# Performance work log

Measured on AMD Instinct MI355X. Metric: run time of the kernel, lower is better.

Reference implementation:

```python
import jax, jax.numpy as jnp
import numpy as np

B, S, H, L, NH, DH, V, FF, WD, W = 16, 512, 768, 12, 12, 64, 30522, 3072, 256, 255
T = S - 1


def layer_norm(x, s, b, eps=1e-12):
    m = jnp.mean(x, -1, keepdims=True)
    v = jnp.mean((x - m) ** 2, -1, keepdims=True)
    return (x - m) * jax.lax.rsqrt(v + eps) * s + b


def setup_inputs() -> dict:
    key = jax.random.key(0)
    ks = jax.random.split(key, 20)
    rng = np.random.RandomState(0)
    # ragged structure: words per sentence and wordpieces per word
    sent_lens = rng.randint(128, W + 1, size=B)
    token_lens = np.zeros((B, W), dtype=np.int32)
    for i in range(B):
        token_lens[i, : sent_lens[i]] = rng.randint(1, 3, size=sent_lens[i])
    bert_len = token_lens.sum(1)  # wordpieces per sentence (no CLS/SEP)
    attention_mask = (np.arange(S)[None, :] < (bert_len + 2)[:, None]).astype(np.int32)
    input_ids = rng.randint(0, V, size=(B, S)).astype(np.int32)
    sd = 0.02
    rn = lambda k, sh: jax.random.normal(k, sh, jnp.float32) * sd
    inp = {
        "input_ids": jnp.asarray(input_ids),
        "attention_mask": jnp.asarray(attention_mask),
        "token_lens": jnp.asarray(token_lens),
        "word_emb": rn(ks[0], (V, H)),
        "pos_emb": rn(ks[1], (S, H)),
        "type_emb": rn(ks[2], (2, H)),
        "emb_ln_s": jnp.ones((H,), jnp.float32),
        "emb_ln_b": jnp.zeros((H,), jnp.float32),
        "Wq": rn(ks[3], (L, H, H)), "bq": jnp.zeros((L, H), jnp.float32),
        "Wk": rn(ks[4], (L, H, H)), "bk": jnp.zeros((L, H), jnp.float32),
        "Wv": rn(ks[5], (L, H, H)), "bv": jnp.zeros((L, H), jnp.float32),
        "Wo": rn(ks[6], (L, H, H)), "bo": jnp.zeros((L, H), jnp.float32),
        "ln1_s": jnp.ones((L, H), jnp.float32), "ln1_b": jnp.zeros((L, H), jnp.float32),
        "W1": rn(ks[7], (L, H, FF)), "b1": jnp.zeros((L, FF), jnp.float32),
        "W2": rn(ks[8], (L, FF, H)), "b2": jnp.zeros((L, H), jnp.float32),
        "ln2_s": jnp.ones((L, H), jnp.float32), "ln2_b": jnp.zeros((L, H), jnp.float32),
        "proj_W": rn(ks[9], (H, WD)), "proj_b": jnp.zeros((WD,), jnp.float32),
    }
    return inp


def reference(input_ids, attention_mask, token_lens, word_emb, pos_emb, type_emb,
              emb_ln_s, emb_ln_b, Wq, bq, Wk, bk, Wv, bv, Wo, bo, ln1_s, ln1_b,
              W1, b1, W2, b2, ln2_s, ln2_b, proj_W, proj_b):
    # --- BERT embeddings ---
    h = word_emb[input_ids] + pos_emb[None, :, :] + type_emb[0][None, None, :]
    h = layer_norm(h, emb_ln_s, emb_ln_b)
    att_bias = (1.0 - attention_mask.astype(jnp.float32))[:, None, None, :] * -10000.0

    def block(h, p):
        wq, bq_, wk, bk_, wv, bv_, wo, bo_, l1s, l1b, w1, b1_, w2, b2_, l2s, l2b = p
        q = (h @ wq + bq_).reshape(B, S, NH, DH)
        k = (h @ wk + bk_).reshape(B, S, NH, DH)
        v = (h @ wv + bv_).reshape(B, S, NH, DH)
        scores = jnp.einsum('bqnd,bknd->bnqk', q, k) / np.float32(np.sqrt(DH)) + att_bias
        a = jax.nn.softmax(scores, axis=-1)
        ctx = jnp.einsum('bnqk,bknd->bqnd', a, v).reshape(B, S, H)
        h = layer_norm(h + ctx @ wo + bo_, l1s, l1b)
        f = jax.nn.gelu(h @ w1 + b1_, approximate=False) @ w2 + b2_
        h = layer_norm(h + f, l2s, l2b)
        return h, None

    h, _ = jax.lax.scan(block, h, (Wq, bq, Wk, bk, Wv, bv, Wo, bo, ln1_s, ln1_b,
                                   W1, b1, W2, b2, ln2_s, ln2_b))
    # drop [CLS], project to word_dims
    hid = h[:, 1:, :] @ proj_W + proj_b  # [B, T, WD]
    # --- ragged segment-mean merge (vectorized form of merge_embedding) ---
    cum = jnp.cumsum(token_lens, axis=1)  # [B, W]
    pos = jnp.arange(T)
    word_id = jnp.sum(pos[None, :, None] >= cum[:, None, :], axis=-1)  # token -> word
    valid = pos[None, :] < cum[:, -1][:, None]  # token within bert_len
    onehot = ((word_id[:, :, None] == jnp.arange(W)[None, None, :]) & valid[:, :, None]).astype(hid.dtype)
    sums = jnp.einsum('btw,btd->bwd', onehot, hid)  # [B, W, WD]
    means = sums / jnp.maximum(token_lens, 1)[:, :, None].astype(hid.dtype)
    word_masks = (token_lens > 0).astype(jnp.float32)  # [B, W]
    return means, word_masks
```

## Files before the change

### kernel.cpp

```cpp
#include <hip/hip_runtime.h>
#include <stdint.h>

#define B_ 16
#define S_ 512
#define H_ 768
#define L_ 12
#define NH_ 12
#define DH_ 64
#define FF_ 3072
#define WD_ 256
#define W_ 255
#define MTOK_ (B_*S_)
#define QKVN_ 2304
#define MPADR_ 128

typedef _Float16 f16;
typedef _Float16 f16x8 __attribute__((ext_vector_type(8)));
typedef _Float16 f16x4 __attribute__((ext_vector_type(4)));
typedef _Float16 f16x2 __attribute__((ext_vector_type(2)));
typedef float f32x4 __attribute__((ext_vector_type(4)));

#define SCHED_FENCE() __builtin_amdgcn_sched_barrier(0)

__device__ __forceinline__ float gelu_fast(float x) {
  float u = x * (1.0f + 0.044715f * x * x);
  float e = __expf(-1.5957691216f * u);
  return __fdividef(x, 1.0f + e);
}

__device__ __forceinline__ void gload16(const f16* g, f16* l) {
  __builtin_amdgcn_global_load_lds(
      (const __attribute__((address_space(1))) void*)g,
      (__attribute__((address_space(3))) void*)l, 16, 0, 0);
}

template<int BM, int BN, int ACT, int OUTF16, int BIAS, int QKVW>
__global__ __launch_bounds__(256) void gemm2_k(
    const f16* __restrict__ A, const f16* __restrict__ Bm, void* __restrict__ Cv,
    const float* __restrict__ bias, f16* __restrict__ vTp,
    const int* __restrict__ rowmap, const int* __restrict__ meta,
    int lda, int ldb, int ldc, int K, float scale)
{
  constexpr int MI = BM / 32;
  constexpr int NI = BN / 32;
  constexpr int LPW = BM / 32 + BN / 32;
  const int gx = gridDim.x;
  int flat = blockIdx.y * gx + blockIdx.x;
  const int nlive = (meta[1] / BM) * gx;
  if (flat >= nlive) return;
  {
    int q = nlive >> 3, r = nlive & 7;
    int xcd = flat & 7, idx = flat >> 3;
    flat = (xcd < r ? xcd * (q + 1) : r * (q + 1) + (xcd - r) * q) + idx;
  }
  const int row0 = (flat / gx) * BM;
  const int col0 = (flat % gx) * BN;

  __shared__ __align__(16) f16 lA[2][BM * 64];
  __shared__ __align__(16) f16 lB[2][BN * 64];
  const int lane = threadIdx.x & 63;
  const int wave = threadIdx.x >> 6;
  const int wr = wave >> 1, wc = wave & 1;
  const int srow = lane >> 3;
  const int scol = lane & 7;
  const int cs = scol ^ srow;

  int arow[BM / 32];
#pragma unroll
  for (int i = 0; i < BM / 32; ++i)
    arow[i] = rowmap[row0 + (wave * (BM / 32) + i) * 8 + srow];

  auto stage = [&](int p, int k0) {
#pragma unroll
    for (int i = 0; i < BM / 32; ++i) {
      int seg = wave * (BM / 32) + i;
      gload16(&A[(size_t)arow[i] * lda + k0 + cs * 8], &lA[p][seg * 512]);
    }
#pragma unroll
    for (int i = 0; i < BN / 32; ++i) {
      int seg = wave * (BN / 32) + i;
      gload16(&Bm[(size_t)(col0 + seg * 8 + srow) * ldb + k0 + cs * 8], &lB[p][seg * 512]);
    }
  };

  f32x4 acc[MI][NI] = {};
  const int nt = K >> 6;
  const int rl = lane & 15, g = lane >> 4;
  stage(0, 0);
  if (nt > 1) stage(1, 64);
  for (int t = 0; t < nt; ++t) {
    if (t < nt - 1) { asm volatile("s_waitcnt vmcnt(%0) lgkmcnt(0)" :: "i"(LPW) : "memory"); }
    else            { asm volatile("s_waitcnt vmcnt(0) lgkmcnt(0)" ::: "memory"); }
    SCHED_FENCE();
    __builtin_amdgcn_s_barrier();
    SCHED_FENCE();
    const int p = t & 1;
    __builtin_amdgcn_s_setprio(1);
#pragma unroll
    for (int c = 0; c < 2; ++c) {
      f16x8 af[MI], bf[NI];
#pragma unroll
      for (int mi = 0; mi < MI; ++mi) {
        int r = wr * (MI * 16) + mi * 16 + rl;
        int u = (c * 4 + g) ^ (r & 7);
        af[mi] = *(const f16x8*)&lA[p][r * 64 + u * 8];
      }
#pragma unroll
      for (int ni = 0; ni < NI; ++ni) {
        int r = wc * (NI * 16) + ni * 16 + rl;
        int u = (c * 4 + g) ^ (r & 7);
        bf[ni] = *(const f16x8*)&lB[p][r * 64 + u * 8];
      }
#pragma unroll
      for (int mi = 0; mi < MI; ++mi)
#pragma unroll
        for (int ni = 0; ni < NI; ++ni)
          acc[mi][ni] = __builtin_amdgcn_mfma_f32_16x16x32_f16(af[mi], bf[ni], acc[mi][ni], 0, 0, 0);
    }
    __builtin_amdgcn_s_setprio(0);
    SCHED_FENCE();
    asm volatile("s_waitcnt lgkmcnt(0)" ::: "memory");
    SCHED_FENCE();
    __builtin_amdgcn_s_barrier();
    SCHED_FENCE();
    if (t + 2 < nt) stage(p, (t + 2) * 64);
  }
  const int cl = lane & 15;
  const int rq = (lane >> 4) * 4;
#pragma unroll
  for (int mi = 0; mi < MI; ++mi) {
    const int4 rm4 = *(const int4*)&rowmap[row0 + wr * (MI * 16) + mi * 16 + rq];
    const int rows[4] = { rm4.x, rm4.y, rm4.z, rm4.w };
    const bool contig = (rm4.w == rm4.x + 3) && ((rm4.x & 3) == 0);
#pragma unroll
    for (int ni = 0; ni < NI; ++ni) {
      int col = col0 + wc * (NI * 16) + ni * 16 + cl;
      float bv = 0.f;
      if constexpr (BIAS) bv = bias[col];
      if constexpr (QKVW) {
        if (col >= 2 * H_) {
          int vc = col - 2 * H_;
          int h = vc >> 6, d = vc & 63;
          if (contig) {
            if (rm4.x < MTOK_) {
              int b = rm4.x >> 9, s = rm4.x & (S_ - 1);
              f16x4 o4;
#pragma unroll
              for (int r = 0; r < 4; ++r) o4[r] = (f16)(acc[mi][ni][r] * scale + bv);
              *(f16x4*)&vTp[(((size_t)(b * NH_ + h)) * DH_ + d) * S_ + s] = o4;
            }
          } else {
#pragma unroll
            for (int r = 0; r < 4; ++r) {
              int orow = rows[r];
              if (orow < MTOK_) {
                int b = orow >> 9, s = orow & (S_ - 1);
                vTp[(((size_t)(b * NH_ + h)) * DH_ + d) * S_ + s] = (f16)(acc[mi][ni][r] * scale + bv);
              }
            }
          }
          continue;
        }
      }
#pragma unroll
      for (int r = 0; r < 4; ++r) {
        float v = acc[mi][ni][r] * scale + bv;
        if constexpr (ACT == 1) v = gelu_fast(v);
        if constexpr (OUTF16) {
          ((f16*)Cv)[(size_t)rows[r] * ldc + col] = (f16)v;
        } else {
          ((float*)Cv)[(size_t)rows[r] * ldc + col] = v;
        }
      }
    }
  }
}

__global__ __launch_bounds__(256) void fattn_k(
    const f16* __restrict__ qkv, const f16* __restrict__ vT,
    f16* __restrict__ ctx, const int* __restrict__ lenp)
{
  const int bh = blockIdx.x, qt = blockIdx.y;
  const int b = bh / NH_, h = bh - b * NH_;
  const int L = lenp[b];
  if ((qt << 7) >= L) return;
  const int nkt = (L + 63) >> 6;
  const int lane = threadIdx.x & 63, wave = threadIdx.x >> 6;
  const int rl = lane & 15, g = lane >> 4;
  const int srow = lane >> 3, scol = lane & 7;
  const int cs = scol ^ srow;

  __shared__ __align__(16) f16 lK[2][64 * 64];
  __shared__ __align__(16) f16 lV[2][64 * 64];
  __shared__ __align__(16) f16 lP[128 * 72];

  auto stage = [&](int p, int kt) {
#pragma unroll
    for (int i = 0; i < 2; ++i) {
      int seg = wave * 2 + i;
      int r = seg * 8 + srow;
      gload16(&qkv[((size_t)b * S_ + kt * 64 + r) * QKVN_ + H_ + h * DH_ + cs * 8], &lK[p][seg * 512]);
      gload16(&vT[((size_t)bh * DH_ + r) * S_ + kt * 64 + cs * 8], &lV[p][seg * 512]);
    }
  };

  const size_t qrow0 = (size_t)b * S_ + qt * 128 + wave * 32;
  f16x8 qf[2][2];
#pragma unroll
  for (int bq = 0; bq < 2; ++bq)
#pragma unroll
    for (int kc = 0; kc < 2; ++kc)
      qf[bq][kc] = *(const f16x8*)&qkv[(qrow0 + bq * 16 + rl) * QKVN_ + h * DH_ + kc * 32 + g * 8];

  float lsum[2] = {0.f, 0.f};
  f32x4 accO[2][4] = {};

  stage(0, 0);
  for (int kt = 0; kt < nkt; ++kt) {
    if (kt + 1 < nkt) {
      stage((kt + 1) & 1, kt + 1);
      asm volatile("s_waitcnt vmcnt(4) lgkmcnt(0)" ::: "memory");
    } else {
      asm volatile("s_waitcnt vmcnt(0) lgkmcnt(0)" ::: "memory");
    }
    SCHED_FENCE();
    __builtin_amdgcn_s_barrier();
    SCHED_FENCE();
    const int p = kt & 1;

    f32x4 accS[4][2] = {};
    __builtin_amdgcn_s_setprio(1);
#pragma unroll
    for (int kc = 0; kc < 2; ++kc) {
#pragma unroll
      for (int ak = 0; ak < 4; ++ak) {
        int row = ak * 16 + rl;
        int u = (kc * 4 + g) ^ (row & 7);
        f16x8 kf = *(const f16x8*)&lK[p][row * 64 + u * 8];
#pragma unroll
        for (int bq = 0; bq < 2; ++bq)
          accS[ak][bq] = __builtin_amdgcn_mfma_f32_16x16x32_f16(kf, qf[bq][kc], accS[ak][bq], 0, 0, 0);
      }
    }
    __builtin_amdgcn_s_setprio(0);

    const int kvb = kt * 64 + g * 4;
#pragma unroll
    for (int bq = 0; bq < 2; ++bq) {
      float pv[16];
      float ps = 0.f;
#pragma unroll
      for (int ak = 0; ak < 4; ++ak)
#pragma unroll
        for (int r = 0; r < 4; ++r) {
          float s = accS[ak][bq][r] * 0.125f;
          float pp = (kvb + ak * 16 + r < L) ? __expf(s) : 0.f;
          pv[ak * 4 + r] = pp;
          ps += pp;
        }
      ps += __shfl_xor(ps, 16);
      ps += __shfl_xor(ps, 32);
      lsum[bq] += ps;
      const int qrow = wave * 32 + bq * 16 + rl;
#pragma unroll
      for (int ak = 0; ak < 4; ++ak)
#pragma unroll
        for (int r2 = 0; r2 < 2; ++r2) {
          f16x2 pk = { (f16)pv[ak * 4 + r2 * 2], (f16)pv[ak * 4 + r2 * 2 + 1] };
          *(f16x2*)&lP[qrow * 72 + ak * 16 + g * 4 + r2 * 2] = pk;
        }
    }
    __builtin_amdgcn_s_setprio(1);
#pragma unroll
    for (int kc = 0; kc < 2; ++kc) {
      f16x8 pa[2], vf[4];
#pragma unroll
      for (int aq = 0; aq < 2; ++aq) {
        int prow = wave * 32 + aq * 16 + rl;
        pa[aq] = *(const f16x8*)&lP[prow * 72 + kc * 32 + g * 8];
      }
#pragma unroll
      for (int bd = 0; bd < 4; ++bd) {
        int vrow = bd * 16 + rl;
        int u = (kc * 4 + g) ^ (vrow & 7);
        vf[bd] = *(const f16x8*)&lV[p][vrow * 64 + u * 8];
      }
#pragma unroll
      for (int aq = 0; aq < 2; ++aq)
#pragma unroll
        for (int bd = 0; bd < 4; ++bd)
          accO[aq][bd] = __builtin_amdgcn_mfma_f32_16x16x32_f16(pa[aq], vf[bd], accO[aq][bd], 0, 0, 0);
    }
    __builtin_amdgcn_s_setprio(0);
    SCHED_FENCE();
    asm volatile("s_waitcnt lgkmcnt(0)" ::: "memory");
    SCHED_FENCE();
    __builtin_amdgcn_s_barrier();
    SCHED_FENCE();
  }

  float linv[2] = { 1.f / lsum[0], 1.f / lsum[1] };
  const size_t orow0 = (size_t)b * S_ + qt * 128 + wave * 32;
#pragma unroll
  for (int aq = 0; aq < 2; ++aq)
#pragma unroll
    for (int r = 0; r < 4; ++r) {
      float li = __shfl(linv[aq], (lane & 48) | (g * 4 + r));
      int q = aq * 16 + g * 4 + r;
#pragma unroll
      for (int bd = 0; bd < 4; ++bd)
        ctx[(orow0 + q) * H_ + h * DH_ + bd * 16 + rl] = (f16)(accO[aq][bd][r] * li);
    }
}

template<typename TI>
__global__ __launch_bounds__(256) void transpose_f16_k(
    const TI* __restrict__ in, f16* __restrict__ out,
    int ldin, int ldout, long i1, long o1)
{
  const int z = blockIdx.z;
  in  += (size_t)z * i1;
  out += (size_t)z * o1;
  __shared__ float t[32][33];
  const int kt = blockIdx.y * 32, nt = blockIdx.x * 32;
  const int tx = threadIdx.x & 31, tg = threadIdx.x >> 5;
#pragma unroll
  for (int i = 0; i < 4; ++i) {
    int k = tg * 4 + i;
    t[k][tx] = (float)in[(size_t)(kt + k) * ldin + nt + tx];
  }
  __syncthreads();
#pragma unroll
  for (int i = 0; i < 4; ++i) {
    int n = tg * 4 + i;
    out[(size_t)(nt + n) * ldout + kt + tx] = (f16)t[tx][n];
  }
}

__global__ void bias_cat_k(const float* __restrict__ bq, const float* __restrict__ bk,
                           const float* __restrict__ bv, float* __restrict__ out) {
  const int l = blockIdx.y;
  const int j = blockIdx.x * 256 + threadIdx.x;
  float v = (j < H_) ? bq[l * H_ + j] : (j < 2 * H_) ? bk[l * H_ + j - H_] : bv[l * H_ + j - 2 * H_];
  out[l * QKVN_ + j] = v;
}

__global__ __launch_bounds__(256) void embed_ln_k(
    const int* __restrict__ ids, const float* __restrict__ wemb,
    const float* __restrict__ pemb, const float* __restrict__ temb,
    const float* __restrict__ lns, const float* __restrict__ lnb,
    float* __restrict__ h32, f16* __restrict__ h16)
{
  const int row = blockIdx.x * 4 + (threadIdx.x >> 6);
  const int lane = threadIdx.x & 63;
  const int s = row & (S_ - 1);
  const float4* wp = (const float4*)(wemb + (size_t)ids[row] * H_);
  const float4* pp = (const float4*)(pemb + (size_t)s * H_);
  const float4* tp = (const float4*)temb;
  float4 x[3]; float sm = 0.f, sq = 0.f;
#pragma unroll
  for (int j = 0; j < 3; ++j) {
    int i4 = lane + 64 * j;
    float4 a = wp[i4], bb = pp[i4], c = tp[i4];
    float4 v; v.x = a.x + bb.x + c.x; v.y = a.y + bb.y + c.y;
    v.z = a.z + bb.z + c.z; v.w = a.w + bb.w + c.w;
    x[j] = v;
    sm += v.x + v.y + v.z + v.w;
    sq += v.x * v.x + v.y * v.y + v.z * v.z + v.w * v.w;
  }
#pragma unroll
  for (int o = 32; o > 0; o >>= 1) { sm += __shfl_xor(sm, o); sq += __shfl_xor(sq, o); }
  float mean = sm * (1.f / H_);
  float inv = rsqrtf(sq * (1.f / H_) - mean * mean + 1e-12f);
  float4* hw = (float4*)(h32 + (size_t)row * H_);
  f16* ho = h16 + (size_t)row * H_;
#pragma unroll
  for (int j = 0; j < 3; ++j) {
    int i4 = lane + 64 * j;
    float4 sc = ((const float4*)lns)[i4], bi = ((const float4*)lnb)[i4];
    float4 v = x[j], y;
    y.x = (v.x - mean) * inv * sc.x + bi.x;
    y.y = (v.y - mean) * inv * sc.y + bi.y;
    y.z = (v.z - mean) * inv * sc.z + bi.z;
    y.w = (v.w - mean) * inv * sc.w + bi.w;
    hw[i4] = y;
    f16x4 o4 = {(f16)y.x, (f16)y.y, (f16)y.z, (f16)y.w};
    *(f16x4*)&ho[i4 * 4] = o4;
  }
}

__global__ __launch_bounds__(256) void ln_res_k(
    float* __restrict__ h32, const f16* __restrict__ tmp,
    const float* __restrict__ lns, const float* __restrict__ lnb,
    f16* __restrict__ h16, const int* __restrict__ rowmap, const int* __restrict__ meta)
{
  const int crow = blockIdx.x * 4 + (threadIdx.x >> 6);
  if (crow >= meta[0]) return;
  const int row = rowmap[crow];
  const int lane = threadIdx.x & 63;
  const float4* hp = (const float4*)(h32 + (size_t)row * H_);
  const f16x4* tp = (const f16x4*)(tmp + (size_t)row * H_);
  float4 x[3]; float sm = 0.f, sq = 0.f;
#pragma unroll
  for (int j = 0; j < 3; ++j) {
    int i4 = lane + 64 * j;
    float4 a = hp[i4];
    f16x4 tv = tp[i4];
    float4 v; v.x = a.x + (float)tv[0]; v.y = a.y + (float)tv[1];
    v.z = a.z + (float)tv[2]; v.w = a.w + (float)tv[3];
    x[j] = v;
    sm += v.x + v.y + v.z + v.w;
    sq += v.x * v.x + v.y * v.y + v.z * v.z + v.w * v.w;
  }
#pragma unroll
  for (int o = 32; o > 0; o >>= 1) { sm += __shfl_xor(sm, o); sq += __shfl_xor(sq, o); }
  float mean = sm * (1.f / H_);
  float inv = rsqrtf(sq * (1.f / H_) - mean * mean + 1e-12f);
  float4* hw = (float4*)(h32 + (size_t)row * H_);
  f16* ho = h16 + (size_t)row * H_;
#pragma unroll
  for (int j = 0; j < 3; ++j) {
    int i4 = lane + 64 * j;
    float4 sc = ((const float4*)lns)[i4], bi = ((const float4*)lnb)[i4];
    float4 v = x[j], y;
    y.x = (v.x - mean) * inv * sc.x + bi.x;
    y.y = (v.y - mean) * inv * sc.y + bi.y;
    y.z = (v.z - mean) * inv * sc.z + bi.z;
    y.w = (v.w - mean) * inv * sc.w + bi.w;
    hw[i4] = y;
    f16x4 o4 = {(f16)y.x, (f16)y.y, (f16)y.z, (f16)y.w};
    *(f16x4*)&ho[i4 * 4] = o4;
  }
}

__global__ void len_k(const int* __restrict__ mask, int* __restrict__ len) {
  const int b = blockIdx.x;
  const int t = threadIdx.x;
  __shared__ int red[512];
  red[t] = mask[b * S_ + t]; __syncthreads();
  for (int o = 256; o > 0; o >>= 1) { if (t < o) red[t] += red[t + o]; __syncthreads(); }
  if (t == 0) len[b] = red[0];
}

__global__ void rowmap_k(const int* __restrict__ len, int* __restrict__ meta,
                         int* __restrict__ rowmap) {
  __shared__ int cum[17];
  if (threadIdx.x == 0) {
    int c = 0; cum[0] = 0;
    for (int b = 0; b < B_; ++b) { c += len[b]; cum[b + 1] = c; }
    meta[0] = c;
    meta[1] = (c + 127) & ~127;
  }
  __syncthreads();
  const int Mv = cum[16];
  for (int i = threadIdx.x; i < MTOK_ + MPADR_; i += 256) {
    int orig;
    if (i < Mv) {
      int b = 0;
#pragma unroll
      for (int t = 1; t <= 16; ++t) b += (i >= cum[t]) ? 1 : 0;
      orig = b * S_ + (i - cum[b]);
    } else {
      int d = i - Mv;
      orig = MTOK_ + (d < MPADR_ ? d : MPADR_ - 1);
    }
    rowmap[i] = orig;
  }
}

__global__ __launch_bounds__(256) void merge_k(
    const float* __restrict__ proj, const int* __restrict__ tl,
    float* __restrict__ means, float* __restrict__ masks)
{
  const int w = blockIdx.x, b = blockIdx.y;
  const int t = threadIdx.x;
  __shared__ int red[256];
  int part = 0;
  for (int j = t; j < w; j += 256) part += tl[b * W_ + j];
  red[t] = part; __syncthreads();
  for (int o = 128; o > 0; o >>= 1) { if (t < o) red[t] += red[t + o]; __syncthreads(); }
  const int start = red[0];
  const int len = tl[b * W_ + w];
  float s = 0.f;
  for (int l = 0; l < len; ++l)
    s += proj[((size_t)b * S_ + 1 + start + l) * WD_ + t];
  means[((size_t)b * W_ + w) * WD_ + t] = (len > 0) ? s / (float)len : 0.f;
  if (t == 0) masks[b * W_ + w] = (len > 0) ? 1.f : 0.f;
}

extern "C" void kernel_launch(void* const* d_in, const int* in_sizes, int n_in,
                              void* d_out, int out_size, void* d_ws, size_t ws_size,
                              hipStream_t stream)
{
  (void)in_sizes; (void)n_in; (void)out_size;
  const int*   ids   = (const int*)d_in[0];
  const int*   amask = (const int*)d_in[1];
  const int*   tlens = (const int*)d_in[2];
  const float* wemb  = (const float*)d_in[3];
  const float* pemb  = (const float*)d_in[4];
  const float* temb  = (const float*)d_in[5];
  const float* elns  = (const float*)d_in[6];
  const float* elnb  = (const float*)d_in[7];
  const float* Wq = (const float*)d_in[8];  const float* bq = (const float*)d_in[9];
  const float* Wk = (const float*)d_in[10]; const float* bk = (const float*)d_in[11];
  const float* Wv = (const float*)d_in[12]; const float* bv = (const float*)d_in[13];
  const float* Wo = (const float*)d_in[14]; const float* bo = (const float*)d_in[15];
  const float* l1s = (const float*)d_in[16]; const float* l1b = (const float*)d_in[17];
  const float* W1 = (const float*)d_in[18]; const float* b1 = (const float*)d_in[19];
  const float* W2 = (const float*)d_in[20]; const float* b2 = (const float*)d_in[21];
  const float* l2s = (const float*)d_in[22]; const float* l2b = (const float*)d_in[23];
  const float* pW = (const float*)d_in[24]; const float* pb = (const float*)d_in[25];

  const int MR = MTOK_ + MPADR_;
  char* ws = (char*)d_ws;
  size_t off = 0;
  auto alloc = [&](size_t n) { void* r = ws + off; off += (n + 255) & ~(size_t)255; return r; };
  float* h32   = (float*)alloc((size_t)MR * H_ * 4);
  f16*   h16   = (f16*)alloc((size_t)MR * H_ * 2);
  f16*   qkv   = (f16*)alloc((size_t)MR * QKVN_ * 2);
  f16*   ctx16 = (f16*)alloc((size_t)MR * H_ * 2);
  f16*   vT    = (f16*)alloc((size_t)B_ * NH_ * DH_ * S_ * 2);
  f16*   ff16  = (f16*)alloc((size_t)MR * FF_ * 2);
  f16*   tmp16 = (f16*)alloc((size_t)MR * H_ * 2);
  float* proj32 = (float*)alloc((size_t)MR * WD_ * 4);
  f16*   pwT   = (f16*)alloc((size_t)WD_ * H_ * 2);
  float* bqkv  = (float*)alloc((size_t)L_ * QKVN_ * 4);
  int*   lenb  = (int*)alloc(256);
  int*   meta  = (int*)alloc(256);
  int*   rowmap = (int*)alloc((size_t)MR * 4);

  const size_t wqkv_sz = (size_t)QKVN_ * H_ * 2;
  const size_t wo_sz   = (size_t)H_ * H_ * 2;
  const size_t w1_sz   = (size_t)H_ * FF_ * 2;
  const size_t w2_sz   = (size_t)FF_ * H_ * 2;
  const size_t per_layer_w = wqkv_sz + wo_sz + w1_sz + w2_sz;
  const bool big = ws_size >= off + (size_t)L_ * per_layer_w + 8192;
  const int nz = big ? L_ : 1;
  f16* wqkv0 = (f16*)alloc((size_t)nz * wqkv_sz);
  f16* wo0   = (f16*)alloc((size_t)nz * wo_sz);
  f16* w10   = (f16*)alloc((size_t)nz * w1_sz);
  f16* w20   = (f16*)alloc((size_t)nz * w2_sz);

  len_k<<<B_, 512, 0, stream>>>(amask, lenb);
  rowmap_k<<<1, 256, 0, stream>>>(lenb, meta, rowmap);
  embed_ln_k<<<MTOK_ / 4, 256, 0, stream>>>(ids, wemb, pemb, temb, elns, elnb, h32, h16);
  transpose_f16_k<float><<<dim3(WD_/32, H_/32, 1), 256, 0, stream>>>(pW, pwT, WD_, H_, 0, 0);
  bias_cat_k<<<dim3(QKVN_/256, L_), 256, 0, stream>>>(bq, bk, bv, bqkv);

  if (big) {
    transpose_f16_k<float><<<dim3(H_/32, H_/32, L_), 256, 0, stream>>>(
        Wq, wqkv0,                   H_, H_, (long)H_*H_, (long)QKVN_*H_);
    transpose_f16_k<float><<<dim3(H_/32, H_/32, L_), 256, 0, stream>>>(
        Wk, wqkv0 + (size_t)H_*H_,   H_, H_, (long)H_*H_, (long)QKVN_*H_);
    transpose_f16_k<float><<<dim3(H_/32, H_/32, L_), 256, 0, stream>>>(
        Wv, wqkv0 + (size_t)2*H_*H_, H_, H_, (long)H_*H_, (long)QKVN_*H_);
    transpose_f16_k<float><<<dim3(H_/32, H_/32, L_), 256, 0, stream>>>(
        Wo, wo0, H_, H_, (long)H_*H_, (long)H_*H_);
    transpose_f16_k<float><<<dim3(FF_/32, H_/32, L_), 256, 0, stream>>>(
        W1, w10, FF_, H_, (long)H_*FF_, (long)H_*FF_);
    transpose_f16_k<float><<<dim3(H_/32, FF_/32, L_), 256, 0, stream>>>(
        W2, w20, H_, FF_, (long)FF_*H_, (long)FF_*H_);
  }

  for (int l = 0; l < L_; ++l) {
    f16* wqkv_l = wqkv0 + (size_t)(big ? l : 0) * QKVN_ * H_;
    f16* wo_l   = wo0   + (size_t)(big ? l : 0) * H_ * H_;
    f16* w1_l   = w10   + (size_t)(big ? l : 0) * H_ * FF_;
    f16* w2_l   = w20   + (size_t)(big ? l : 0) * FF_ * H_;
    if (!big) {
      transpose_f16_k<float><<<dim3(H_/32, H_/32, 1), 256, 0, stream>>>(
          Wq + (size_t)l*H_*H_, wqkv_l,                   H_, H_, 0, 0);
      transpose_f16_k<float><<<dim3(H_/32, H_/32, 1), 256, 0, stream>>>(
          Wk + (size_t)l*H_*H_, wqkv_l + (size_t)H_*H_,   H_, H_, 0, 0);
      transpose_f16_k<float><<<dim3(H_/32, H_/32, 1), 256, 0, stream>>>(
          Wv + (size_t)l*H_*H_, wqkv_l + (size_t)2*H_*H_, H_, H_, 0, 0);
      transpose_f16_k<float><<<dim3(H_/32, H_/32, 1), 256, 0, stream>>>(
          Wo + (size_t)l*H_*H_, wo_l, H_, H_, 0, 0);
      transpose_f16_k<float><<<dim3(FF_/32, H_/32, 1), 256, 0, stream>>>(
          W1 + (size_t)l*H_*FF_, w1_l, FF_, H_, 0, 0);
      transpose_f16_k<float><<<dim3(H_/32, FF_/32, 1), 256, 0, stream>>>(
          W2 + (size_t)l*FF_*H_, w2_l, H_, FF_, 0, 0);
    }
    gemm2_k<64,128,0,1,1,1><<<dim3(QKVN_/128, MTOK_/64, 1), 256, 0, stream>>>(
        h16, wqkv_l, qkv, bqkv + (size_t)l*QKVN_, vT, rowmap, meta, H_, H_, QKVN_, H_, 1.0f);
    fattn_k<<<dim3(B_*NH_, S_/128), 256, 0, stream>>>(qkv, vT, ctx16, lenb);
    gemm2_k<64,64,0,1,1,0><<<dim3(H_/64, MTOK_/64, 1), 256, 0, stream>>>(
        ctx16, wo_l, tmp16, bo + (size_t)l*H_, nullptr, rowmap, meta, H_, H_, H_, H_, 1.0f);
    ln_res_k<<<MTOK_/4, 256, 0, stream>>>(h32, tmp16, l1s + (size_t)l*H_, l1b + (size_t)l*H_, h16, rowmap, meta);
    gemm2_k<64,128,1,1,1,0><<<dim3(FF_/128, MTOK_/64, 1), 256, 0, stream>>>(
        h16, w1_l, ff16, b1 + (size_t)l*FF_, nullptr, rowmap, meta, H_, H_, FF_, H_, 1.0f);
    gemm2_k<64,64,0,1,1,0><<<dim3(H_/64, MTOK_/64, 1), 256, 0, stream>>>(
        ff16, w2_l, tmp16, b2 + (size_t)l*H_, nullptr, rowmap, meta, FF_, FF_, H_, FF_, 1.0f);
    ln_res_k<<<MTOK_/4, 256, 0, stream>>>(h32, tmp16, l2s + (size_t)l*H_, l2b + (size_t)l*H_, h16, rowmap, meta);
  }

  gemm2_k<64,64,0,0,1,0><<<dim3(WD_/64, MTOK_/64, 1), 256, 0, stream>>>(
      h16, pwT, proj32, pb, nullptr, rowmap, meta, H_, H_, WD_, H_, 1.0f);
  merge_k<<<dim3(W_, B_), 256, 0, stream>>>(proj32, tlens,
      (float*)d_out, (float*)d_out + (size_t)B_ * W_ * WD_);
}
```

Measured before the change: 2.369 ms.

## Split-K the N=768 GEMMs and enlarge QKV/FFN1 tiles to 128x128

Adds a SPLITK template parameter to the GEMM kernel. The Wo and W2 projections (N=768) now run with 64x128 tiles split two ways along K, each half writing its own f16 partial buffer. The residual LayerNorm kernel then sums both partials, and only the first split adds the bias. The QKV and FFN1 GEMMs move to 128x128 tiles for more data reuse per block. The aim is better occupancy for the narrow-N GEMMs and less redundant loading in the wide ones, at the cost of an extra partial-sum buffer write and read and fewer blocks for the large GEMMs.

```diff
diff --git a/kernel.cpp b/kernel.cpp
--- a/kernel.cpp
+++ b/kernel.cpp
@@ -34,12 +34,12 @@
       (__attribute__((address_space(3))) void*)l, 16, 0, 0);
 }
 
-template<int BM, int BN, int ACT, int OUTF16, int BIAS, int QKVW>
+template<int BM, int BN, int ACT, int OUTF16, int BIAS, int QKVW, int SPLITK>
 __global__ __launch_bounds__(256) void gemm2_k(
     const f16* __restrict__ A, const f16* __restrict__ Bm, void* __restrict__ Cv,
     const float* __restrict__ bias, f16* __restrict__ vTp,
     const int* __restrict__ rowmap, const int* __restrict__ meta,
-    int lda, int ldb, int ldc, int K, float scale)
+    int lda, int ldb, int ldc, int K, float scale, long czoff)
 {
   constexpr int MI = BM / 32;
   constexpr int NI = BN / 32;
@@ -55,6 +55,10 @@
   }
   const int row0 = (flat / gx) * BM;
   const int col0 = (flat % gx) * BN;
+  const int z = (SPLITK > 1) ? blockIdx.z : 0;
+  const int kc_len = K / SPLITK;
+  A  += (size_t)z * kc_len;
+  Bm += (size_t)z * kc_len;
 
   __shared__ __align__(16) f16 lA[2][BM * 64];
   __shared__ __align__(16) f16 lB[2][BN * 64];
@@ -84,7 +88,7 @@
   };
 
   f32x4 acc[MI][NI] = {};
-  const int nt = K >> 6;
+  const int nt = kc_len >> 6;
   const int rl = lane & 15, g = lane >> 4;
   stage(0, 0);
   if (nt > 1) stage(1, 64);
@@ -136,7 +140,7 @@
     for (int ni = 0; ni < NI; ++ni) {
       int col = col0 + wc * (NI * 16) + ni * 16 + cl;
       float bv = 0.f;
-      if constexpr (BIAS) bv = bias[col];
+      if constexpr (BIAS) { if (SPLITK == 1 || z == 0) bv = bias[col]; }
       if constexpr (QKVW) {
         if (col >= 2 * H_) {
           int vc = col - 2 * H_;
@@ -167,7 +171,7 @@
         float v = acc[mi][ni][r] * scale + bv;
         if constexpr (ACT == 1) v = gelu_fast(v);
         if constexpr (OUTF16) {
-          ((f16*)Cv)[(size_t)rows[r] * ldc + col] = (f16)v;
+          ((f16*)Cv + (size_t)z * czoff)[(size_t)rows[r] * ldc + col] = (f16)v;
         } else {
           ((float*)Cv)[(size_t)rows[r] * ldc + col] = v;
         }
@@ -390,7 +394,7 @@
 }
 
 __global__ __launch_bounds__(256) void ln_res_k(
-    float* __restrict__ h32, const f16* __restrict__ tmp,
+    float* __restrict__ h32, const f16* __restrict__ tmpA, const f16* __restrict__ tmpB,
     const float* __restrict__ lns, const float* __restrict__ lnb,
     f16* __restrict__ h16, const int* __restrict__ rowmap, const int* __restrict__ meta)
 {
@@ -399,15 +403,19 @@
   const int row = rowmap[crow];
   const int lane = threadIdx.x & 63;
   const float4* hp = (const float4*)(h32 + (size_t)row * H_);
-  const f16x4* tp = (const f16x4*)(tmp + (size_t)row * H_);
+  const f16x4* ta = (const f16x4*)(tmpA + (size_t)row * H_);
+  const f16x4* tb = (const f16x4*)(tmpB + (size_t)row * H_);
   float4 x[3]; float sm = 0.f, sq = 0.f;
 #pragma unroll
   for (int j = 0; j < 3; ++j) {
     int i4 = lane + 64 * j;
     float4 a = hp[i4];
-    f16x4 tv = tp[i4];
-    float4 v; v.x = a.x + (float)tv[0]; v.y = a.y + (float)tv[1];
-    v.z = a.z + (float)tv[2]; v.w = a.w + (float)tv[3];
+    f16x4 va = ta[i4], vb = tb[i4];
+    float4 v;
+    v.x = a.x + (float)va[0] + (float)vb[0];
+    v.y = a.y + (float)va[1] + (float)vb[1];
+    v.z = a.z + (float)va[2] + (float)vb[2];
+    v.w = a.w + (float)va[3] + (float)vb[3];
     x[j] = v;
     sm += v.x + v.y + v.z + v.w;
     sq += v.x * v.x + v.y * v.y + v.z * v.z + v.w * v.w;
@@ -521,13 +529,14 @@
   f16*   ctx16 = (f16*)alloc((size_t)MR * H_ * 2);
   f16*   vT    = (f16*)alloc((size_t)B_ * NH_ * DH_ * S_ * 2);
   f16*   ff16  = (f16*)alloc((size_t)MR * FF_ * 2);
-  f16*   tmp16 = (f16*)alloc((size_t)MR * H_ * 2);
+  f16*   tmp16 = (f16*)alloc((size_t)MR * H_ * 2 * 2);
   float* proj32 = (float*)alloc((size_t)MR * WD_ * 4);
   f16*   pwT   = (f16*)alloc((size_t)WD_ * H_ * 2);
   float* bqkv  = (float*)alloc((size_t)L_ * QKVN_ * 4);
   int*   lenb  = (int*)alloc(256);
   int*   meta  = (int*)alloc(256);
   int*   rowmap = (int*)alloc((size_t)MR * 4);
+  f16*   tmp16b = tmp16 + (size_t)MR * H_;
 
   const size_t wqkv_sz = (size_t)QKVN_ * H_ * 2;
   const size_t wo_sz   = (size_t)H_ * H_ * 2;
@@ -581,21 +590,21 @@
       transpose_f16_k<float><<<dim3(H_/32, FF_/32, 1), 256, 0, stream>>>(
           W2 + (size_t)l*FF_*H_, w2_l, H_, FF_, 0, 0);
     }
-    gemm2_k<64,128,0,1,1,1><<<dim3(QKVN_/128, MTOK_/64, 1), 256, 0, stream>>>(
-        h16, wqkv_l, qkv, bqkv + (size_t)l*QKVN_, vT, rowmap, meta, H_, H_, QKVN_, H_, 1.0f);
+    gemm2_k<128,128,0,1,1,1,1><<<dim3(QKVN_/128, MTOK_/128, 1), 256, 0, stream>>>(
+        h16, wqkv_l, qkv, bqkv + (size_t)l*QKVN_, vT, rowmap, meta, H_, H_, QKVN_, H_, 1.0f, 0);
     fattn_k<<<dim3(B_*NH_, S_/128), 256, 0, stream>>>(qkv, vT, ctx16, lenb);
-    gemm2_k<64,64,0,1,1,0><<<dim3(H_/64, MTOK_/64, 1), 256, 0, stream>>>(
-        ctx16, wo_l, tmp16, bo + (size_t)l*H_, nullptr, rowmap, meta, H_, H_, H_, H_, 1.0f);
-    ln_res_k<<<MTOK_/4, 256, 0, stream>>>(h32, tmp16, l1s + (size_t)l*H_, l1b + (size_t)l*H_, h16, rowmap, meta);
-    gemm2_k<64,128,1,1,1,0><<<dim3(FF_/128, MTOK_/64, 1), 256, 0, stream>>>(
-        h16, w1_l, ff16, b1 + (size_t)l*FF_, nullptr, rowmap, meta, H_, H_, FF_, H_, 1.0f);
-    gemm2_k<64,64,0,1,1,0><<<dim3(H_/64, MTOK_/64, 1), 256, 0, stream>>>(
-        ff16, w2_l, tmp16, b2 + (size_t)l*H_, nullptr, rowmap, meta, FF_, FF_, H_, FF_, 1.0f);
-    ln_res_k<<<MTOK_/4, 256, 0, stream>>>(h32, tmp16, l2s + (size_t)l*H_, l2b + (size_t)l*H_, h16, rowmap, meta);
-  }
-
-  gemm2_k<64,64,0,0,1,0><<<dim3(WD_/64, MTOK_/64, 1), 256, 0, stream>>>(
-      h16, pwT, proj32, pb, nullptr, rowmap, meta, H_, H_, WD_, H_, 1.0f);
+    gemm2_k<64,128,0,1,1,0,2><<<dim3(H_/128, MTOK_/64, 2), 256, 0, stream>>>(
+        ctx16, wo_l, tmp16, bo + (size_t)l*H_, nullptr, rowmap, meta, H_, H_, H_, H_, 1.0f, (long)MR * H_);
+    ln_res_k<<<MTOK_/4, 256, 0, stream>>>(h32, tmp16, tmp16b, l1s + (size_t)l*H_, l1b + (size_t)l*H_, h16, rowmap, meta);
+    gemm2_k<128,128,1,1,1,0,1><<<dim3(FF_/128, MTOK_/128, 1), 256, 0, stream>>>(
+        h16, w1_l, ff16, b1 + (size_t)l*FF_, nullptr, rowmap, meta, H_, H_, FF_, H_, 1.0f, 0);
+    gemm2_k<64,128,0,1,1,0,2><<<dim3(H_/128, MTOK_/64, 2), 256, 0, stream>>>(
+        ff16, w2_l, tmp16, b2 + (size_t)l*H_, nullptr, rowmap, meta, FF_, FF_, H_, FF_, 1.0f, (long)MR * H_);
+    ln_res_k<<<MTOK_/4, 256, 0, stream>>>(h32, tmp16, tmp16b, l2s + (size_t)l*H_, l2b + (size_t)l*H_, h16, rowmap, meta);
+  }
+
+  gemm2_k<64,64,0,0,1,0,1><<<dim3(WD_/64, MTOK_/64, 1), 256, 0, stream>>>(
+      h16, pwT, proj32, pb, nullptr, rowmap, meta, H_, H_, WD_, H_, 1.0f, 0);
   merge_k<<<dim3(W_, B_), 256, 0, stream>>>(proj32, tlens,
       (float*)d_out, (float*)d_out + (size_t)B_ * W_ * WD_);
 }
```

Measured after the change: 2.476 ms. 1.05x slower.

## Drop GEMM double-buffered prefetch and use 128x128 tiles for QKV and FFN1

Applied to the files above, without the earlier changes.

Replaces the two-stage LDS double buffer, with its manual vmcnt waits and priority hints, by a single-buffer load-sync-compute loop using __syncthreads. This halves the LDS footprint per block. The QKV and FFN1 GEMMs switch from 64x128 to 128x128 tiles to raise data reuse per block. In exchange, global loads no longer overlap MFMA work and each K step pays two full barriers, which risks exposing memory latency.

```diff
diff --git a/kernel.cpp b/kernel.cpp
--- a/kernel.cpp
+++ b/kernel.cpp
@@ -43,7 +43,6 @@
 {
   constexpr int MI = BM / 32;
   constexpr int NI = BN / 32;
-  constexpr int LPW = BM / 32 + BN / 32;
   const int gx = gridDim.x;
   int flat = blockIdx.y * gx + blockIdx.x;
   const int nlive = (meta[1] / BM) * gx;
@@ -56,8 +55,8 @@
   const int row0 = (flat / gx) * BM;
   const int col0 = (flat % gx) * BN;
 
-  __shared__ __align__(16) f16 lA[2][BM * 64];
-  __shared__ __align__(16) f16 lB[2][BN * 64];
+  __shared__ __align__(16) f16 lA[BM * 64];
+  __shared__ __align__(16) f16 lB[BN * 64];
   const int lane = threadIdx.x & 63;
   const int wave = threadIdx.x >> 6;
   const int wr = wave >> 1, wc = wave & 1;
@@ -70,32 +69,23 @@
   for (int i = 0; i < BM / 32; ++i)
     arow[i] = rowmap[row0 + (wave * (BM / 32) + i) * 8 + srow];
 
-  auto stage = [&](int p, int k0) {
-#pragma unroll
-    for (int i = 0; i < BM / 32; ++i) {
-      int seg = wave * (BM / 32) + i;
-      gload16(&A[(size_t)arow[i] * lda + k0 + cs * 8], &lA[p][seg * 512]);
-    }
-#pragma unroll
-    for (int i = 0; i < BN / 32; ++i) {
-      int seg = wave * (BN / 32) + i;
-      gload16(&Bm[(size_t)(col0 + seg * 8 + srow) * ldb + k0 + cs * 8], &lB[p][seg * 512]);
-    }
-  };
-
   f32x4 acc[MI][NI] = {};
   const int nt = K >> 6;
   const int rl = lane & 15, g = lane >> 4;
-  stage(0, 0);
-  if (nt > 1) stage(1, 64);
   for (int t = 0; t < nt; ++t) {
-    if (t < nt - 1) { asm volatile("s_waitcnt vmcnt(%0) lgkmcnt(0)" :: "i"(LPW) : "memory"); }
-    else            { asm volatile("s_waitcnt vmcnt(0) lgkmcnt(0)" ::: "memory"); }
-    SCHED_FENCE();
-    __builtin_amdgcn_s_barrier();
-    SCHED_FENCE();
-    const int p = t & 1;
-    __builtin_amdgcn_s_setprio(1);
+    __syncthreads();
+    const int k0 = t * 64;
+#pragma unroll
+    for (int i = 0; i < BM / 32; ++i) {
+      int seg = wave * (BM / 32) + i;
+      gload16(&A[(size_t)arow[i] * lda + k0 + cs * 8], &lA[seg * 512]);
+    }
+#pragma unroll
+    for (int i = 0; i < BN / 32; ++i) {
+      int seg = wave * (BN / 32) + i;
+      gload16(&Bm[(size_t)(col0 + seg * 8 + srow) * ldb + k0 + cs * 8], &lB[seg * 512]);
+    }
+    __syncthreads();
 #pragma unroll
     for (int c = 0; c < 2; ++c) {
       f16x8 af[MI], bf[NI];
@@ -103,13 +93,13 @@
       for (int mi = 0; mi < MI; ++mi) {
         int r = wr * (MI * 16) + mi * 16 + rl;
         int u = (c * 4 + g) ^ (r & 7);
-        af[mi] = *(const f16x8*)&lA[p][r * 64 + u * 8];
+        af[mi] = *(const f16x8*)&lA[r * 64 + u * 8];
       }
 #pragma unroll
       for (int ni = 0; ni < NI; ++ni) {
         int r = wc * (NI * 16) + ni * 16 + rl;
         int u = (c * 4 + g) ^ (r & 7);
-        bf[ni] = *(const f16x8*)&lB[p][r * 64 + u * 8];
+        bf[ni] = *(const f16x8*)&lB[r * 64 + u * 8];
       }
 #pragma unroll
       for (int mi = 0; mi < MI; ++mi)
@@ -117,13 +107,6 @@
         for (int ni = 0; ni < NI; ++ni)
           acc[mi][ni] = __builtin_amdgcn_mfma_f32_16x16x32_f16(af[mi], bf[ni], acc[mi][ni], 0, 0, 0);
     }
-    __builtin_amdgcn_s_setprio(0);
-    SCHED_FENCE();
-    asm volatile("s_waitcnt lgkmcnt(0)" ::: "memory");
-    SCHED_FENCE();
-    __builtin_amdgcn_s_barrier();
-    SCHED_FENCE();
-    if (t + 2 < nt) stage(p, (t + 2) * 64);
   }
   const int cl = lane & 15;
   const int rq = (lane >> 4) * 4;
@@ -581,13 +564,13 @@
       transpose_f16_k<float><<<dim3(H_/32, FF_/32, 1), 256, 0, stream>>>(
           W2 + (size_t)l*FF_*H_, w2_l, H_, FF_, 0, 0);
     }
-    gemm2_k<64,128,0,1,1,1><<<dim3(QKVN_/128, MTOK_/64, 1), 256, 0, stream>>>(
+    gemm2_k<128,128,0,1,1,1><<<dim3(QKVN_/128, MTOK_/128, 1), 256, 0, stream>>>(
         h16, wqkv_l, qkv, bqkv + (size_t)l*QKVN_, vT, rowmap, meta, H_, H_, QKVN_, H_, 1.0f);
     fattn_k<<<dim3(B_*NH_, S_/128), 256, 0, stream>>>(qkv, vT, ctx16, lenb);
     gemm2_k<64,64,0,1,1,0><<<dim3(H_/64, MTOK_/64, 1), 256, 0, stream>>>(
         ctx16, wo_l, tmp16, bo + (size_t)l*H_, nullptr, rowmap, meta, H_, H_, H_, H_, 1.0f);
     ln_res_k<<<MTOK_/4, 256, 0, stream>>>(h32, tmp16, l1s + (size_t)l*H_, l1b + (size_t)l*H_, h16, rowmap, meta);
-    gemm2_k<64,128,1,1,1,0><<<dim3(FF_/128, MTOK_/64, 1), 256, 0, stream>>>(
+    gemm2_k<128,128,1,1,1,0><<<dim3(FF_/128, MTOK_/128, 1), 256, 0, stream>>>(
         h16, w1_l, ff16, b1 + (size_t)l*FF_, nullptr, rowmap, meta, H_, H_, FF_, H_, 1.0f);
     gemm2_k<64,64,0,1,1,0><<<dim3(H_/64, MTOK_/64, 1), 256, 0, stream>>>(
         ff16, w2_l, tmp16, b2 + (size_t)l*H_, nullptr, rowmap, meta, FF_, FF_, H_, FF_, 1.0f);
```

Result: no change. 2.344 ms (-1.1%).
